# Optimization experiments

Hardware: AMD Instinct MI355X
Metric: run time of the kernel (lower is better)

The kernel has to match this reference:

```python
import jax, jax.numpy as jnp
import numpy as np

NHEADS = 16
RANK = 8


def _rope(t):
    # t: (B, H, S, hd); past_len = 0 (no kv cache)
    hd = t.shape[-1]
    S = t.shape[2]
    inv = 1.0 / (10000.0 ** (jnp.arange(0, hd, 2, dtype=jnp.float32) / hd))  # (hd/2,)
    ang = jnp.arange(S, dtype=jnp.float32)[:, None] * inv[None, :]           # (S, hd/2)
    cos = jnp.concatenate([jnp.cos(ang), jnp.cos(ang)], -1)[None, None]      # (1,1,S,hd)
    sin = jnp.concatenate([jnp.sin(ang), jnp.sin(ang)], -1)[None, None]
    t1, t2 = jnp.split(t, 2, axis=-1)
    rot = jnp.concatenate([-t2, t1], -1)
    return t * cos + rot * sin


def _hyper_linear(x, Ws, bs, w1, b1, w2, b2, gA_w, gA_b, gB_w, gB_b):
    # Static path + per-batch dynamic low-rank correction generated from pooled context.
    B, S, D = x.shape
    z = x.mean(axis=1)                              # (B, D) pooled context
    h = jax.nn.silu(z @ w1 + b1)                    # (B, D/ratio)
    c = h @ w2 + b2                                 # (B, dynamic_dim)
    A = (c @ gA_w + gA_b).reshape(B, RANK, D)       # (B, rank, D_in)
    Bm = (c @ gB_w + gB_b).reshape(B, D, RANK)      # (B, D_out, rank)
    xa = jnp.einsum('bsd,brd->bsr', x, A)           # (B, S, rank)
    dyn = jnp.einsum('bsr,bor->bso', xa, Bm) / RANK # (B, S, D_out)
    return x @ Ws + bs + dyn


def _forward(x, Wq, bq, Wo, bo,
             Wk, bk, k_w1, k_b1, k_w2, k_b2, k_gA_w, k_gA_b, k_gB_w, k_gB_b,
             Wv, bv, v_w1, v_b1, v_w2, v_b2, v_gA_w, v_gA_b, v_gB_w, v_gB_b):
    B, S, D = x.shape
    hd = D // NHEADS
    q = x @ Wq + bq
    k = _hyper_linear(x, Wk, bk, k_w1, k_b1, k_w2, k_b2, k_gA_w, k_gA_b, k_gB_w, k_gB_b)
    v = _hyper_linear(x, Wv, bv, v_w1, v_b1, v_w2, v_b2, v_gA_w, v_gA_b, v_gB_w, v_gB_b)
    # (B, S, D) -> (B, H, S, hd)
    q = q.reshape(B, S, NHEADS, hd).transpose(0, 2, 1, 3)
    k = k.reshape(B, S, NHEADS, hd).transpose(0, 2, 1, 3)
    v = v.reshape(B, S, NHEADS, hd).transpose(0, 2, 1, 3)
    q = _rope(q)
    k = _rope(k)
    # causal SDPA (kv_cache is None -> is_causal=True)
    scale = 1.0 / jnp.sqrt(jnp.asarray(hd, dtype=x.dtype))
    scores = jnp.einsum('bhqd,bhkd->bhqk', q, k) * scale
    mask = jnp.tril(jnp.ones((S, S), dtype=bool))
    scores = jnp.where(mask, scores, jnp.asarray(-1e30, dtype=scores.dtype))
    attn = jax.nn.softmax(scores, axis=-1)
    out = jnp.einsum('bhqk,bhkd->bhqd', attn, v)
    out = out.transpose(0, 2, 1, 3).reshape(B, S, D)
    return out @ Wo + bo


def setup_inputs() -> dict:
    key = jax.random.key(0)
    D, HID, DYN = 1024, 256, 64
    B, S = 2, 2048
    ks = jax.random.split(key, 32)
    w = lambda i, shp: jax.random.normal(ks[i], shp, dtype=jnp.float32) * 0.02
    inp = {
        'x': jax.random.normal(ks[0], (B, S, D), dtype=jnp.float32),
        'Wq': w(1, (D, D)), 'bq': jnp.zeros((D,), jnp.float32),
        'Wo': w(2, (D, D)), 'bo': jnp.zeros((D,), jnp.float32),
        'Wk': w(3, (D, D)), 'bk': jnp.zeros((D,), jnp.float32),
        'k_w1': w(4, (D, HID)), 'k_b1': jnp.zeros((HID,), jnp.float32),
        'k_w2': w(5, (HID, DYN)), 'k_b2': jnp.zeros((DYN,), jnp.float32),
        'k_gA_w': w(6, (DYN, RANK * D)), 'k_gA_b': jnp.zeros((RANK * D,), jnp.float32),
        'k_gB_w': w(7, (DYN, D * RANK)), 'k_gB_b': jnp.zeros((D * RANK,), jnp.float32),
        'Wv': w(8, (D, D)), 'bv': jnp.zeros((D,), jnp.float32),
        'v_w1': w(9, (D, HID)), 'v_b1': jnp.zeros((HID,), jnp.float32),
        'v_w2': w(10, (HID, DYN)), 'v_b2': jnp.zeros((DYN,), jnp.float32),
        'v_gA_w': w(11, (DYN, RANK * D)), 'v_gA_b': jnp.zeros((RANK * D,), jnp.float32),
        'v_gB_w': w(12, (DYN, D * RANK)), 'v_gB_b': jnp.zeros((D * RANK,), jnp.float32),
    }
    return inp


def reference(x, Wq, bq, Wo, bo,
              Wk, bk, k_w1, k_b1, k_w2, k_b2, k_gA_w, k_gA_b, k_gB_w, k_gB_b,
              Wv, bv, v_w1, v_b1, v_w2, v_b2, v_gA_w, v_gA_b, v_gB_w, v_gB_b):
    return _forward(x, Wq, bq, Wo, bo,
                    Wk, bk, k_w1, k_b1, k_w2, k_b2, k_gA_w, k_gA_b, k_gB_w, k_gB_b,
                    Wv, bv, v_w1, v_b1, v_w2, v_b2, v_gA_w, v_gA_b, v_gB_w, v_gB_b)
```

## Files before the change

kernel.cpp:

```cpp
#include <hip/hip_runtime.h>
#include <math.h>

#define BB 2
#define SS 2048
#define DD 1024
#define NH 16
#define HDM 64
#define RNK 8

typedef short short8 __attribute__((ext_vector_type(8)));
typedef float floatx4 __attribute__((ext_vector_type(4)));

static __device__ __forceinline__ ushort f2bf(float f) {
  union { float f; unsigned u; } v;
  v.f = f;
  unsigned r = (v.u + 0x7FFFu + ((v.u >> 16) & 1u)) >> 16;
  return (ushort)r;
}
static __device__ __forceinline__ float bf2f(ushort u) {
  union { unsigned u; float f; } v;
  v.u = ((unsigned)u) << 16;
  return v.f;
}

__global__ __launch_bounds__(256) void z_pool(const float* __restrict__ x,
                                              float* __restrict__ zsum) {
  int b = blockIdx.x;
  int s0 = blockIdx.y * 16;
  int tid = threadIdx.x;
  float p0 = 0.f, p1 = 0.f, p2 = 0.f, p3 = 0.f;
  const float* xp = x + ((size_t)b * SS + s0) * DD;
  for (int s = 0; s < 16; ++s) {
    const float* row = xp + (size_t)s * DD;
    p0 += row[tid];
    p1 += row[tid + 256];
    p2 += row[tid + 512];
    p3 += row[tid + 768];
  }
  atomicAdd(&zsum[b * DD + tid], p0);
  atomicAdd(&zsum[b * DD + tid + 256], p1);
  atomicAdd(&zsum[b * DD + tid + 512], p2);
  atomicAdd(&zsum[b * DD + tid + 768], p3);
}

__global__ __launch_bounds__(256) void gen_h(
    const float* __restrict__ zsum,
    const float* __restrict__ kw1, const float* __restrict__ vw1,
    float* __restrict__ h_pre) {
  int b = blockIdx.x & 1;
  int p = (blockIdx.x >> 1) & 1;
  int slice = blockIdx.y;
  const float* w1 = p ? vw1 : kw1;
  int tid = threadIdx.x;
  float acc = 0.f;
  int j0 = slice * 128;
  for (int j = j0; j < j0 + 128; ++j) {
    float z = zsum[b * DD + j] * (1.0f / (float)SS);
    acc += z * w1[j * 256 + tid];
  }
  atomicAdd(&h_pre[(p * 2 + b) * 256 + tid], acc);
}

__global__ __launch_bounds__(256) void hyper_c2(
    const float* __restrict__ h_pre,
    const float* __restrict__ kb1, const float* __restrict__ kw2,
    const float* __restrict__ kb2,
    const float* __restrict__ vb1, const float* __restrict__ vw2,
    const float* __restrict__ vb2, float* __restrict__ c_all) {
  int p = blockIdx.x >> 1;
  int b = blockIdx.x & 1;
  const float* b1 = p ? vb1 : kb1;
  const float* w2 = p ? vw2 : kw2;
  const float* b2 = p ? vb2 : kb2;
  __shared__ float hs[256];
  __shared__ float part[256];
  int tid = threadIdx.x;
  float hv = h_pre[(p * 2 + b) * 256 + tid] + b1[tid];
  hs[tid] = hv / (1.0f + expf(-hv));
  __syncthreads();
  int n = tid & 63, chunk = tid >> 6;
  float a = 0.f;
  for (int jj = 0; jj < 64; ++jj) {
    int j = chunk * 64 + jj;
    a += hs[j] * w2[j * 64 + n];
  }
  part[tid] = a;
  __syncthreads();
  if (tid < 64) {
    c_all[(p * 2 + b) * 64 + tid] =
        part[tid] + part[tid + 64] + part[tid + 128] + part[tid + 192] + b2[tid];
  }
}

__global__ __launch_bounds__(256) void gen_AB(
    const float* __restrict__ c_all,
    const float* __restrict__ kgAw, const float* __restrict__ kgAb,
    const float* __restrict__ kgBw, const float* __restrict__ kgBb,
    const float* __restrict__ vgAw, const float* __restrict__ vgAb,
    const float* __restrict__ vgBw, const float* __restrict__ vgBb,
    float* __restrict__ Ak, float* __restrict__ Bk,
    float* __restrict__ Av, float* __restrict__ Bv) {
  int y = blockIdx.y;
  int p = y >> 1, mat = y & 1;
  const float* gw = p ? (mat ? vgBw : vgAw) : (mat ? kgBw : kgAw);
  const float* gb = p ? (mat ? vgBb : vgAb) : (mat ? kgBb : kgAb);
  float* obase = p ? (mat ? Bv : Av) : (mat ? Bk : Ak);

  __shared__ float c0[64], c1[64];
  int tid = threadIdx.x;
  if (tid < 64) c0[tid] = c_all[p * 128 + tid];
  else if (tid < 128) c1[tid - 64] = c_all[p * 128 + tid];
  __syncthreads();

  int idx = blockIdx.x * 256 + tid;
  float a0 = gb[idx], a1 = a0;
#pragma unroll
  for (int j = 0; j < 64; ++j) {
    float w = gw[j * (RNK * DD) + idx];
    a0 += c0[j] * w;
    a1 += c1[j] * w;
  }
  obase[idx] = a0;
  obase[RNK * DD + idx] = a1;
}

__global__ __launch_bounds__(256) void cvt_bf16(const float* __restrict__ in,
                                                ushort* __restrict__ out) {
  int gid = blockIdx.x * 256 + threadIdx.x;
  float4 a = ((const float4*)in)[gid];
  ushort4 o;
  o.x = f2bf(a.x);
  o.y = f2bf(a.y);
  o.z = f2bf(a.z);
  o.w = f2bf(a.w);
  ((ushort4*)out)[gid] = o;
}

__global__ __launch_bounds__(256) void cvt_wt(const float* __restrict__ W,
                                              ushort* __restrict__ Wt) {
  __shared__ float tile[32][33];
  int bx = blockIdx.x, by = blockIdx.y;
  int tx = threadIdx.x & 31, ty = threadIdx.x >> 5;
#pragma unroll
  for (int i = 0; i < 4; ++i)
    tile[ty + 8 * i][tx] = W[(size_t)(by * 32 + ty + 8 * i) * DD + bx * 32 + tx];
  __syncthreads();
#pragma unroll
  for (int i = 0; i < 4; ++i)
    Wt[(size_t)(bx * 32 + ty + 8 * i) * DD + by * 32 + tx] =
        f2bf(tile[tx][ty + 8 * i]);
}

__global__ __launch_bounds__(256) void rope_tab(float2* __restrict__ tab) {
  int gid = blockIdx.x * 256 + threadIdx.x;
  int i = gid >> 11, s = gid & 2047;
  float freq = expf(-(float)i * (9.210340371976184f / 32.0f));
  float sn, cn;
  sincosf((float)s * freq, &sn, &cn);
  tab[gid] = make_float2(cn, sn);
}

__global__ __launch_bounds__(256) void weff(
    const float* __restrict__ Ak, const float* __restrict__ Bk,
    const float* __restrict__ Av, const float* __restrict__ Bv,
    const ushort* __restrict__ Wtk, const ushort* __restrict__ Wtv,
    ushort* __restrict__ Wcat) {
  int y = blockIdx.y;
  int p = y >> 1, b = y & 1;
  const float* A = (p ? Av : Ak) + b * (RNK * DD);
  const float* Bm = (p ? Bv : Bk) + b * (RNK * DD);
  const ushort* src = p ? Wtv : Wtk;
  ushort* dst = Wcat + ((size_t)(1 + 2 * p + b) << 20);

  int tid = threadIdx.x;
  int row = blockIdx.x * 16 + (tid >> 4);
  int cg = tid & 15;
  float bm[RNK];
#pragma unroll
  for (int r = 0; r < RNK; ++r) bm[r] = Bm[row * RNK + r];
  for (int kk = cg * 64; kk < cg * 64 + 64; kk += 4) {
    float4 acc = make_float4(0.f, 0.f, 0.f, 0.f);
#pragma unroll
    for (int r = 0; r < RNK; ++r) {
      float4 a4 = *(const float4*)&A[r * DD + kk];
      acc.x += bm[r] * a4.x;
      acc.y += bm[r] * a4.y;
      acc.z += bm[r] * a4.z;
      acc.w += bm[r] * a4.w;
    }
    ushort4 ws = *(const ushort4*)&src[(size_t)row * DD + kk];
    ushort4 o;
    o.x = f2bf(bf2f(ws.x) + acc.x * 0.125f);
    o.y = f2bf(bf2f(ws.y) + acc.y * 0.125f);
    o.z = f2bf(bf2f(ws.z) + acc.z * 0.125f);
    o.w = f2bf(bf2f(ws.w) + acc.w * 0.125f);
    *(ushort4*)&dst[(size_t)row * DD + kk] = o;
  }
}

__global__ __launch_bounds__(256) void gemm_qkv(
    const ushort* __restrict__ Axb, const ushort* __restrict__ Wcat,
    const float* __restrict__ bq, const float* __restrict__ bk,
    const float* __restrict__ bv, const float2* __restrict__ tab,
    ushort* __restrict__ qhb, ushort* __restrict__ khb,
    ushort* __restrict__ vhb) {
  __shared__ ushort As[128][40];
  __shared__ ushort Bs[128][40];
  int tid = threadIdx.x;
  int bm = blockIdx.x * 128;
  int ny = blockIdx.y;
  int path = ny >> 3;
  int nb = (ny & 7) * 128;
  int b_blk = bm >> 11;
  const ushort* Wbase =
      (path == 0) ? Wcat : Wcat + ((size_t)(1 + (path - 1) * 2 + b_blk) << 20);
  const float* bias = (path == 0) ? bq : (path == 1 ? bk : bv);
  ushort* outp = (path == 0) ? qhb : (path == 1 ? khb : vhb);

  int w = tid >> 6, lane = tid & 63, l16 = lane & 15, q4 = lane >> 4;
  int wm = (w >> 1) * 64, wn = (w & 1) * 64;
  floatx4 acc[4][4];
#pragma unroll
  for (int mi = 0; mi < 4; ++mi)
#pragma unroll
    for (int ni = 0; ni < 4; ++ni) acc[mi][ni] = 0;

  int sr = tid >> 2, sc = (tid & 3) * 8;
  const ushort* Ap0 = Axb + (size_t)(bm + sr) * DD + sc;
  const ushort* Ap1 = Axb + (size_t)(bm + sr + 64) * DD + sc;
  const ushort* Bp0 = Wbase + (size_t)(nb + sr) * DD + sc;
  const ushort* Bp1 = Wbase + (size_t)(nb + sr + 64) * DD + sc;

  for (int k0 = 0; k0 < DD; k0 += 32) {
    uint4 a0 = *(const uint4*)(Ap0 + k0);
    uint4 a1 = *(const uint4*)(Ap1 + k0);
    uint4 b0 = *(const uint4*)(Bp0 + k0);
    uint4 b1 = *(const uint4*)(Bp1 + k0);
    __syncthreads();
    *(uint4*)&As[sr][sc] = a0;
    *(uint4*)&As[sr + 64][sc] = a1;
    *(uint4*)&Bs[sr][sc] = b0;
    *(uint4*)&Bs[sr + 64][sc] = b1;
    __syncthreads();
    short8 af[4], bf[4];
#pragma unroll
    for (int mi = 0; mi < 4; ++mi)
      af[mi] = *(const short8*)&As[wm + mi * 16 + l16][q4 * 8];
#pragma unroll
    for (int ni = 0; ni < 4; ++ni)
      bf[ni] = *(const short8*)&Bs[wn + ni * 16 + l16][q4 * 8];
#pragma unroll
    for (int mi = 0; mi < 4; ++mi)
#pragma unroll
      for (int ni = 0; ni < 4; ++ni)
        acc[mi][ni] = __builtin_amdgcn_mfma_f32_16x16x32_bf16(
            af[mi], bf[ni], acc[mi][ni], 0, 0, 0);
  }

  int h = (nb + wn) >> 6;
  float biasv[4];
#pragma unroll
  for (int ni = 0; ni < 4; ++ni) biasv[ni] = bias[nb + wn + ni * 16 + l16];

#pragma unroll
  for (int mi = 0; mi < 4; ++mi) {
#pragma unroll
    for (int r = 0; r < 4; ++r) {
      int grow = bm + wm + mi * 16 + q4 * 4 + r;
      int bb = grow >> 11, s = grow & 2047;
      ushort* orow = outp + (((size_t)(bb * NH + h) * SS + s) << 6);
      float v[4];
#pragma unroll
      for (int ni = 0; ni < 4; ++ni) v[ni] = acc[mi][ni][r] + biasv[ni];
      if (path < 2) {
#pragma unroll
        for (int ni = 0; ni < 2; ++ni) {
          float2 cs = tab[((ni * 16 + l16) << 11) + s];
          float a = v[ni] * cs.x - v[ni + 2] * cs.y;
          float c = v[ni + 2] * cs.x + v[ni] * cs.y;
          v[ni] = a;
          v[ni + 2] = c;
        }
      }
#pragma unroll
      for (int ni = 0; ni < 4; ++ni) orow[ni * 16 + l16] = f2bf(v[ni]);
    }
  }
}

#define VT_IDX(d, c) ((unsigned)(72 * (d) + 16 * ((d) >> 3) + (c)))

__global__ __launch_bounds__(256) void attn_mfma2(
    const ushort* __restrict__ qh, const ushort* __restrict__ kh,
    const ushort* __restrict__ vh, ushort* __restrict__ ao) {
  __shared__ ushort Ks[64][72];
  __shared__ ushort Vt[4720];
  __shared__ ushort Ps[128][72];
  int bid = blockIdx.x;
  int bh = bid & 31;
  int q0 = (15 - (bid >> 5)) * 128;
  int b = bh >> 4, h = bh & 15;
  int tid = threadIdx.x;
  int w = tid >> 6, lane = tid & 63, l16 = lane & 15, q4 = lane >> 4;

  short8 qf[2][2];
#pragma unroll
  for (int mi = 0; mi < 2; ++mi) {
    const ushort* qrow =
        qh + ((size_t)bh * SS + q0 + 32 * w + mi * 16 + l16) * HDM;
    qf[mi][0] = *(const short8*)(qrow + q4 * 8);
    qf[mi][1] = *(const short8*)(qrow + 32 + q4 * 8);
  }

  floatx4 o[2][4];
#pragma unroll
  for (int mi = 0; mi < 2; ++mi)
#pragma unroll
    for (int ni = 0; ni < 4; ++ni) o[mi][ni] = 0;
  float l_part[2][4] = {};

  int nkt = (q0 >> 6) + 2;
  int skr = tid >> 2, skc = (tid & 3) * 8;
  int so8 = tid & 7, sp = tid >> 3;
  const ushort* kbase = kh + (size_t)bh * SS * HDM;
  const ushort* vbase = vh + (size_t)bh * SS * HDM;

  for (int kt = 0; kt < nkt; ++kt) {
    int k0 = kt * 64;
    __syncthreads();
    *(uint4*)&Ks[skr][skc] =
        *(const uint4*)(kbase + (size_t)(k0 + skr) * HDM + skc);
    *(uint4*)&Ks[skr][skc + 32] =
        *(const uint4*)(kbase + (size_t)(k0 + skr) * HDM + skc + 32);
    const ushort* v0 = vbase + (size_t)(k0 + 2 * sp) * HDM + so8 * 8;
    uint4 va = *(const uint4*)v0;
    uint4 vb = *(const uint4*)(v0 + HDM);
    const ushort* pa = (const ushort*)&va;
    const ushort* pb = (const ushort*)&vb;
#pragma unroll
    for (int j = 0; j < 8; ++j) {
      int d = so8 * 8 + j;
      *(unsigned*)&Vt[VT_IDX(d, 2 * sp)] =
          (unsigned)pa[j] | ((unsigned)pb[j] << 16);
    }
    __syncthreads();

    floatx4 s4[2][4];
#pragma unroll
    for (int ni = 0; ni < 4; ++ni) {
      short8 kf0 = *(const short8*)&Ks[ni * 16 + l16][q4 * 8];
      short8 kf1 = *(const short8*)&Ks[ni * 16 + l16][32 + q4 * 8];
#pragma unroll
      for (int mi = 0; mi < 2; ++mi) {
        floatx4 c;
        c = 0;
        c = __builtin_amdgcn_mfma_f32_16x16x32_bf16(qf[mi][0], kf0, c, 0, 0, 0);
        c = __builtin_amdgcn_mfma_f32_16x16x32_bf16(qf[mi][1], kf1, c, 0, 0, 0);
        s4[mi][ni] = c;
      }
    }

    bool diag = (kt >= nkt - 2);
#pragma unroll
    for (int mi = 0; mi < 2; ++mi) {
#pragma unroll
      for (int r = 0; r < 4; ++r) {
        int qg = q0 + 32 * w + mi * 16 + q4 * 4 + r;
        int prow = 32 * w + mi * 16 + q4 * 4 + r;
        float lp = 0.f;
#pragma unroll
        for (int ni = 0; ni < 4; ++ni) {
          float t = s4[mi][ni][r] * 0.18033688f;
          if (diag && (k0 + ni * 16 + l16) > qg) t = -1e38f;
          float p = exp2f(t);
          lp += p;
          Ps[prow][ni * 16 + l16] = f2bf(p);
        }
        l_part[mi][r] += lp;
      }
    }

    short8 pf[2][2];
#pragma unroll
    for (int mi = 0; mi < 2; ++mi) {
      pf[mi][0] = *(const short8*)&Ps[32 * w + mi * 16 + l16][q4 * 8];
      pf[mi][1] = *(const short8*)&Ps[32 * w + mi * 16 + l16][32 + q4 * 8];
    }
#pragma unroll
    for (int ni = 0; ni < 4; ++ni) {
      short8 vf0 = *(const short8*)&Vt[VT_IDX(ni * 16 + l16, q4 * 8)];
      short8 vf1 = *(const short8*)&Vt[VT_IDX(ni * 16 + l16, 32 + q4 * 8)];
#pragma unroll
      for (int mi = 0; mi < 2; ++mi) {
        o[mi][ni] =
            __builtin_amdgcn_mfma_f32_16x16x32_bf16(pf[mi][0], vf0, o[mi][ni], 0, 0, 0);
        o[mi][ni] =
            __builtin_amdgcn_mfma_f32_16x16x32_bf16(pf[mi][1], vf1, o[mi][ni], 0, 0, 0);
      }
    }
  }

#pragma unroll
  for (int mi = 0; mi < 2; ++mi) {
#pragma unroll
    for (int r = 0; r < 4; ++r) {
      float l = l_part[mi][r];
      l += __shfl_xor(l, 1);
      l += __shfl_xor(l, 2);
      l += __shfl_xor(l, 4);
      l += __shfl_xor(l, 8);
      float inv = 1.0f / l;
      int token = q0 + 32 * w + mi * 16 + q4 * 4 + r;
      ushort* orow = ao + ((size_t)(b * SS + token)) * DD + h * HDM;
#pragma unroll
      for (int ni = 0; ni < 4; ++ni)
        orow[ni * 16 + l16] = f2bf(o[mi][ni][r] * inv);
    }
  }
}

__global__ __launch_bounds__(256) void gemm_out(
    const ushort* __restrict__ A, const ushort* __restrict__ Bt,
    const float* __restrict__ bias, float* __restrict__ C) {
  __shared__ ushort As[64][40];
  __shared__ ushort Bs[128][40];
  int tid = threadIdx.x;
  int bm = blockIdx.x * 64, bn = blockIdx.y * 128;
  int w = tid >> 6, lane = tid & 63, l16 = lane & 15, q4 = lane >> 4;
  int wm = (w >> 1) * 32, wn = (w & 1) * 64;
  floatx4 acc[2][4];
#pragma unroll
  for (int mi = 0; mi < 2; ++mi)
#pragma unroll
    for (int ni = 0; ni < 4; ++ni) acc[mi][ni] = 0;

  int sr = tid >> 2, sc = (tid & 3) * 8;
  const ushort* Ap0 = A + (size_t)(bm + sr) * DD + sc;
  const ushort* Bp0 = Bt + (size_t)(bn + sr) * DD + sc;
  const ushort* Bp1 = Bt + (size_t)(bn + sr + 64) * DD + sc;

  for (int k0 = 0; k0 < DD; k0 += 32) {
    uint4 a0 = *(const uint4*)(Ap0 + k0);
    uint4 b0 = *(const uint4*)(Bp0 + k0);
    uint4 b1 = *(const uint4*)(Bp1 + k0);
    __syncthreads();
    *(uint4*)&As[sr & 63][sc] = a0;
    *(uint4*)&Bs[sr][sc] = b0;
    *(uint4*)&Bs[sr + 64][sc] = b1;
    __syncthreads();
    short8 af[2], bf[4];
#pragma unroll
    for (int mi = 0; mi < 2; ++mi)
      af[mi] = *(const short8*)&As[wm + mi * 16 + l16][q4 * 8];
#pragma unroll
    for (int ni = 0; ni < 4; ++ni)
      bf[ni] = *(const short8*)&Bs[wn + ni * 16 + l16][q4 * 8];
#pragma unroll
    for (int mi = 0; mi < 2; ++mi)
#pragma unroll
      for (int ni = 0; ni < 4; ++ni)
        acc[mi][ni] = __builtin_amdgcn_mfma_f32_16x16x32_bf16(
            af[mi], bf[ni], acc[mi][ni], 0, 0, 0);
  }
#pragma unroll
  for (int mi = 0; mi < 2; ++mi) {
#pragma unroll
    for (int r = 0; r < 4; ++r) {
      int row = bm + wm + mi * 16 + q4 * 4 + r;
      float* Cr = C + (size_t)row * DD;
#pragma unroll
      for (int ni = 0; ni < 4; ++ni) {
        int col = bn + wn + ni * 16 + l16;
        Cr[col] = acc[mi][ni][r] + bias[col];
      }
    }
  }
}

extern "C" void kernel_launch(void* const* d_in, const int* in_sizes, int n_in,
                              void* d_out, int out_size, void* d_ws,
                              size_t ws_size, hipStream_t stream) {
  const float* x    = (const float*)d_in[0];
  const float* Wq   = (const float*)d_in[1];
  const float* bq   = (const float*)d_in[2];
  const float* Wo   = (const float*)d_in[3];
  const float* bo   = (const float*)d_in[4];
  const float* Wk   = (const float*)d_in[5];
  const float* bk   = (const float*)d_in[6];
  const float* kw1  = (const float*)d_in[7];
  const float* kb1  = (const float*)d_in[8];
  const float* kw2  = (const float*)d_in[9];
  const float* kb2  = (const float*)d_in[10];
  const float* kgAw = (const float*)d_in[11];
  const float* kgAb = (const float*)d_in[12];
  const float* kgBw = (const float*)d_in[13];
  const float* kgBb = (const float*)d_in[14];
  const float* Wv   = (const float*)d_in[15];
  const float* bv   = (const float*)d_in[16];
  const float* vw1  = (const float*)d_in[17];
  const float* vb1  = (const float*)d_in[18];
  const float* vw2  = (const float*)d_in[19];
  const float* vb2  = (const float*)d_in[20];
  const float* vgAw = (const float*)d_in[21];
  const float* vgAb = (const float*)d_in[22];
  const float* vgBw = (const float*)d_in[23];
  const float* vgBb = (const float*)d_in[24];
  float* out = (float*)d_out;

  char* ws = (char*)d_ws;
  const size_t MB = 1024 * 1024;
  ushort* qhb  = (ushort*)(ws);
  ushort* khb  = (ushort*)(ws + 8 * MB);
  ushort* vhb  = (ushort*)(ws + 16 * MB);
  ushort* xb   = (ushort*)(ws + 24 * MB);
  ushort* aob  = (ushort*)(ws + 32 * MB);
  ushort* Wcat = (ushort*)(ws + 40 * MB);
  ushort* Wto  = (ushort*)(ws + 50 * MB);
  ushort* Wtk  = (ushort*)(ws + 52 * MB);
  ushort* Wtv  = (ushort*)(ws + 54 * MB);
  float*  Ak   = (float*)(ws + 56 * MB);
  float*  Bk   = Ak + BB * RNK * DD;
  float*  Av   = Bk + BB * RNK * DD;
  float*  Bv   = Av + BB * RNK * DD;
  float*  zsum = Bv + BB * RNK * DD;
  float*  h_pre = zsum + BB * DD;
  float*  c_all = h_pre + 4 * 256;
  float2* tab  = (float2*)(ws + 56 * MB + 512 * 1024);

  hipMemsetAsync(zsum, 0, (BB * DD + 4 * 256) * sizeof(float), stream);
  z_pool<<<dim3(BB, SS / 16), 256, 0, stream>>>(x, zsum);
  gen_h<<<dim3(4, 8), 256, 0, stream>>>(zsum, kw1, vw1, h_pre);
  hyper_c2<<<4, 256, 0, stream>>>(h_pre, kb1, kw2, kb2, vb1, vw2, vb2, c_all);
  gen_AB<<<dim3(RNK * DD / 256, 4), 256, 0, stream>>>(
      c_all, kgAw, kgAb, kgBw, kgBb, vgAw, vgAb, vgBw, vgBb, Ak, Bk, Av, Bv);

  cvt_bf16<<<(BB * SS * DD / 4) / 256, 256, 0, stream>>>(x, xb);
  cvt_wt<<<dim3(32, 32), 256, 0, stream>>>(Wq, Wcat);
  cvt_wt<<<dim3(32, 32), 256, 0, stream>>>(Wk, Wtk);
  cvt_wt<<<dim3(32, 32), 256, 0, stream>>>(Wv, Wtv);
  cvt_wt<<<dim3(32, 32), 256, 0, stream>>>(Wo, Wto);
  rope_tab<<<(32 * 2048) / 256, 256, 0, stream>>>(tab);
  weff<<<dim3(64, 4), 256, 0, stream>>>(Ak, Bk, Av, Bv, Wtk, Wtv, Wcat);

  gemm_qkv<<<dim3(32, 24), 256, 0, stream>>>(xb, Wcat, bq, bk, bv, tab, qhb,
                                             khb, vhb);
  attn_mfma2<<<512, 256, 0, stream>>>(qhb, khb, vhb, aob);
  gemm_out<<<dim3(64, 8), 256, 0, stream>>>(aob, Wto, bo, out);
}
```

Before: 335.4 us.

## Rewrite attention kernel with 64-row tiles, register K, and double-buffered V

Replaces the attention kernel with a 128-thread version over 64-query tiles, launching twice as many blocks. K fragments now load straight into registers and V goes into a double-buffered transposed LDS tile, with the next tile prefetched during compute so there is one barrier per iteration instead of two. The MFMA operands are swapped (K·Q, V·P) so results land in a layout that allows packed P and output stores. P is rounded to bf16 by truncation rather than round-to-nearest, which adds a small precision risk.

```diff
diff --git a/kernel.cpp b/kernel.cpp
--- a/kernel.cpp
+++ b/kernel.cpp
@@ -21,6 +21,20 @@
   union { unsigned u; float f; } v;
   v.u = ((unsigned)u) << 16;
   return v.f;
+}
+static __device__ __forceinline__ unsigned pack_bf_trunc(float a, float b) {
+  union { float f; unsigned u; } x, y;
+  x.f = a;
+  y.f = b;
+  return __builtin_amdgcn_perm(y.u, x.u, 0x07060302u);
+}
+static __device__ __forceinline__ unsigned pack_bf_rne(float a, float b) {
+  union { float f; unsigned u; } x, y;
+  x.f = a;
+  y.f = b;
+  unsigned xu = x.u + 0x7FFFu + ((x.u >> 16) & 1u);
+  unsigned yu = y.u + 0x7FFFu + ((y.u >> 16) & 1u);
+  return __builtin_amdgcn_perm(yu, xu, 0x07060302u);
 }
 
 __global__ __launch_bounds__(256) void z_pool(const float* __restrict__ x,
@@ -290,131 +304,170 @@
 
 #define VT_IDX(d, c) ((unsigned)(72 * (d) + 16 * ((d) >> 3) + (c)))
 
-__global__ __launch_bounds__(256) void attn_mfma2(
+__global__ __launch_bounds__(128) void attn_mfma3(
     const ushort* __restrict__ qh, const ushort* __restrict__ kh,
     const ushort* __restrict__ vh, ushort* __restrict__ ao) {
-  __shared__ ushort Ks[64][72];
-  __shared__ ushort Vt[4720];
-  __shared__ ushort Ps[128][72];
+  __shared__ ushort Ps[64][72];
+  __shared__ ushort Vt[2][4720];
   int bid = blockIdx.x;
   int bh = bid & 31;
-  int q0 = (15 - (bid >> 5)) * 128;
+  int q0 = (31 - (bid >> 5)) * 64;
   int b = bh >> 4, h = bh & 15;
   int tid = threadIdx.x;
   int w = tid >> 6, lane = tid & 63, l16 = lane & 15, q4 = lane >> 4;
-
-  short8 qf[2][2];
-#pragma unroll
-  for (int mi = 0; mi < 2; ++mi) {
-    const ushort* qrow =
-        qh + ((size_t)bh * SS + q0 + 32 * w + mi * 16 + l16) * HDM;
-    qf[mi][0] = *(const short8*)(qrow + q4 * 8);
-    qf[mi][1] = *(const short8*)(qrow + 32 + q4 * 8);
-  }
-
-  floatx4 o[2][4];
-#pragma unroll
-  for (int mi = 0; mi < 2; ++mi)
-#pragma unroll
-    for (int ni = 0; ni < 4; ++ni) o[mi][ni] = 0;
-  float l_part[2][4] = {};
-
-  int nkt = (q0 >> 6) + 2;
-  int skr = tid >> 2, skc = (tid & 3) * 8;
-  int so8 = tid & 7, sp = tid >> 3;
+  int nkt = (q0 >> 6) + 1;
+
   const ushort* kbase = kh + (size_t)bh * SS * HDM;
   const ushort* vbase = vh + (size_t)bh * SS * HDM;
 
+  short8 qf[2][2];
+#pragma unroll
+  for (int qi = 0; qi < 2; ++qi) {
+    const ushort* qrow = qh + ((size_t)bh * SS + q0 + 32 * w + 16 * qi + l16) * HDM;
+    qf[qi][0] = *(const short8*)(qrow + 8 * q4);
+    qf[qi][1] = *(const short8*)(qrow + 32 + 8 * q4);
+  }
+
+  int so8 = tid & 7, sp = (tid >> 3) & 15;
+
+  short8 kf[4][2];
+#pragma unroll
+  for (int ki = 0; ki < 4; ++ki) {
+    const ushort* kr = kbase + (size_t)(16 * ki + l16) * HDM + 8 * q4;
+    kf[ki][0] = *(const short8*)(kr);
+    kf[ki][1] = *(const short8*)(kr + 32);
+  }
+  uint4 vr[4];
+#pragma unroll
+  for (int j = 0; j < 4; ++j)
+    vr[j] = *(const uint4*)(vbase + (size_t)(4 * sp + j) * HDM + 8 * so8);
+#pragma unroll
+  for (int j = 0; j < 4; j += 2) {
+    const ushort* pa = (const ushort*)&vr[j];
+    const ushort* pb = (const ushort*)&vr[j + 1];
+#pragma unroll
+    for (int dd = 0; dd < 8; ++dd) {
+      int d = so8 * 8 + dd;
+      *(unsigned*)&Vt[0][VT_IDX(d, 4 * sp + j)] =
+          (unsigned)pa[dd] | ((unsigned)pb[dd] << 16);
+    }
+  }
+  __syncthreads();
+
+  floatx4 o[4][2];
+#pragma unroll
+  for (int di = 0; di < 4; ++di)
+#pragma unroll
+    for (int qi = 0; qi < 2; ++qi) o[di][qi] = 0;
+  float l_part[2] = {0.f, 0.f};
+
   for (int kt = 0; kt < nkt; ++kt) {
-    int k0 = kt * 64;
-    __syncthreads();
-    *(uint4*)&Ks[skr][skc] =
-        *(const uint4*)(kbase + (size_t)(k0 + skr) * HDM + skc);
-    *(uint4*)&Ks[skr][skc + 32] =
-        *(const uint4*)(kbase + (size_t)(k0 + skr) * HDM + skc + 32);
-    const ushort* v0 = vbase + (size_t)(k0 + 2 * sp) * HDM + so8 * 8;
-    uint4 va = *(const uint4*)v0;
-    uint4 vb = *(const uint4*)(v0 + HDM);
-    const ushort* pa = (const ushort*)&va;
-    const ushort* pb = (const ushort*)&vb;
-#pragma unroll
-    for (int j = 0; j < 8; ++j) {
-      int d = so8 * 8 + j;
-      *(unsigned*)&Vt[VT_IDX(d, 2 * sp)] =
-          (unsigned)pa[j] | ((unsigned)pb[j] << 16);
-    }
-    __syncthreads();
+    int buf = kt & 1;
+    bool has_next = (kt + 1) < nkt;
+    short8 kn[4][2];
+    if (has_next) {
+      int k0n = (kt + 1) * 64;
+#pragma unroll
+      for (int ki = 0; ki < 4; ++ki) {
+        const ushort* kr = kbase + (size_t)(k0n + 16 * ki + l16) * HDM + 8 * q4;
+        kn[ki][0] = *(const short8*)(kr);
+        kn[ki][1] = *(const short8*)(kr + 32);
+      }
+#pragma unroll
+      for (int j = 0; j < 4; ++j)
+        vr[j] = *(const uint4*)(vbase + (size_t)(k0n + 4 * sp + j) * HDM + 8 * so8);
+    }
 
     floatx4 s4[2][4];
 #pragma unroll
-    for (int ni = 0; ni < 4; ++ni) {
-      short8 kf0 = *(const short8*)&Ks[ni * 16 + l16][q4 * 8];
-      short8 kf1 = *(const short8*)&Ks[ni * 16 + l16][32 + q4 * 8];
-#pragma unroll
-      for (int mi = 0; mi < 2; ++mi) {
+    for (int ki = 0; ki < 4; ++ki)
+#pragma unroll
+      for (int qi = 0; qi < 2; ++qi) {
         floatx4 c;
         c = 0;
-        c = __builtin_amdgcn_mfma_f32_16x16x32_bf16(qf[mi][0], kf0, c, 0, 0, 0);
-        c = __builtin_amdgcn_mfma_f32_16x16x32_bf16(qf[mi][1], kf1, c, 0, 0, 0);
-        s4[mi][ni] = c;
-      }
-    }
-
-    bool diag = (kt >= nkt - 2);
-#pragma unroll
-    for (int mi = 0; mi < 2; ++mi) {
-#pragma unroll
-      for (int r = 0; r < 4; ++r) {
-        int qg = q0 + 32 * w + mi * 16 + q4 * 4 + r;
-        int prow = 32 * w + mi * 16 + q4 * 4 + r;
-        float lp = 0.f;
-#pragma unroll
-        for (int ni = 0; ni < 4; ++ni) {
-          float t = s4[mi][ni][r] * 0.18033688f;
-          if (diag && (k0 + ni * 16 + l16) > qg) t = -1e38f;
-          float p = exp2f(t);
-          lp += p;
-          Ps[prow][ni * 16 + l16] = f2bf(p);
+        c = __builtin_amdgcn_mfma_f32_16x16x32_bf16(kf[ki][0], qf[qi][0], c, 0, 0, 0);
+        c = __builtin_amdgcn_mfma_f32_16x16x32_bf16(kf[ki][1], qf[qi][1], c, 0, 0, 0);
+        s4[qi][ki] = c;
+      }
+
+    bool diag = (kt == nkt - 1);
+#pragma unroll
+    for (int qi = 0; qi < 2; ++qi) {
+      int qloc = 32 * w + 16 * qi + l16;
+      float lp = 0.f;
+#pragma unroll
+      for (int ki = 0; ki < 4; ++ki) {
+        float p[4];
+#pragma unroll
+        for (int r = 0; r < 4; ++r) {
+          float t = s4[qi][ki][r] * 0.18033688f;
+          float pv = exp2f(t);
+          if (diag && (16 * ki + 4 * q4 + r) > qloc) pv = 0.f;
+          p[r] = pv;
+          lp += pv;
         }
-        l_part[mi][r] += lp;
-      }
-    }
-
-    short8 pf[2][2];
-#pragma unroll
-    for (int mi = 0; mi < 2; ++mi) {
-      pf[mi][0] = *(const short8*)&Ps[32 * w + mi * 16 + l16][q4 * 8];
-      pf[mi][1] = *(const short8*)&Ps[32 * w + mi * 16 + l16][32 + q4 * 8];
-    }
-#pragma unroll
-    for (int ni = 0; ni < 4; ++ni) {
-      short8 vf0 = *(const short8*)&Vt[VT_IDX(ni * 16 + l16, q4 * 8)];
-      short8 vf1 = *(const short8*)&Vt[VT_IDX(ni * 16 + l16, 32 + q4 * 8)];
-#pragma unroll
-      for (int mi = 0; mi < 2; ++mi) {
-        o[mi][ni] =
-            __builtin_amdgcn_mfma_f32_16x16x32_bf16(pf[mi][0], vf0, o[mi][ni], 0, 0, 0);
-        o[mi][ni] =
-            __builtin_amdgcn_mfma_f32_16x16x32_bf16(pf[mi][1], vf1, o[mi][ni], 0, 0, 0);
-      }
-    }
-  }
-
-#pragma unroll
-  for (int mi = 0; mi < 2; ++mi) {
-#pragma unroll
-    for (int r = 0; r < 4; ++r) {
-      float l = l_part[mi][r];
-      l += __shfl_xor(l, 1);
-      l += __shfl_xor(l, 2);
-      l += __shfl_xor(l, 4);
-      l += __shfl_xor(l, 8);
-      float inv = 1.0f / l;
-      int token = q0 + 32 * w + mi * 16 + q4 * 4 + r;
-      ushort* orow = ao + ((size_t)(b * SS + token)) * DD + h * HDM;
-#pragma unroll
-      for (int ni = 0; ni < 4; ++ni)
-        orow[ni * 16 + l16] = f2bf(o[mi][ni][r] * inv);
+        unsigned u0 = pack_bf_trunc(p[0], p[1]);
+        unsigned u1 = pack_bf_trunc(p[2], p[3]);
+        uint2 u2;
+        u2.x = u0;
+        u2.y = u1;
+        *(uint2*)&Ps[qloc][16 * ki + 4 * q4] = u2;
+      }
+      l_part[qi] += lp;
+    }
+
+#pragma unroll
+    for (int qi = 0; qi < 2; ++qi) {
+      short8 pf0 = *(const short8*)&Ps[32 * w + 16 * qi + l16][8 * q4];
+      short8 pf1 = *(const short8*)&Ps[32 * w + 16 * qi + l16][32 + 8 * q4];
+#pragma unroll
+      for (int di = 0; di < 4; ++di) {
+        short8 vf0 = *(const short8*)&Vt[buf][VT_IDX(16 * di + l16, 8 * q4)];
+        short8 vf1 = *(const short8*)&Vt[buf][VT_IDX(16 * di + l16, 32 + 8 * q4)];
+        o[di][qi] =
+            __builtin_amdgcn_mfma_f32_16x16x32_bf16(vf0, pf0, o[di][qi], 0, 0, 0);
+        o[di][qi] =
+            __builtin_amdgcn_mfma_f32_16x16x32_bf16(vf1, pf1, o[di][qi], 0, 0, 0);
+      }
+    }
+
+    if (has_next) {
+      int nb = (kt + 1) & 1;
+#pragma unroll
+      for (int j = 0; j < 4; j += 2) {
+        const ushort* pa = (const ushort*)&vr[j];
+        const ushort* pb = (const ushort*)&vr[j + 1];
+#pragma unroll
+        for (int dd = 0; dd < 8; ++dd) {
+          int d = so8 * 8 + dd;
+          *(unsigned*)&Vt[nb][VT_IDX(d, 4 * sp + j)] =
+              (unsigned)pa[dd] | ((unsigned)pb[dd] << 16);
+        }
+      }
+#pragma unroll
+      for (int ki = 0; ki < 4; ++ki) {
+        kf[ki][0] = kn[ki][0];
+        kf[ki][1] = kn[ki][1];
+      }
+    }
+    __syncthreads();
+  }
+
+#pragma unroll
+  for (int qi = 0; qi < 2; ++qi) {
+    float l = l_part[qi];
+    l += __shfl_xor(l, 16);
+    l += __shfl_xor(l, 32);
+    float inv = 1.0f / l;
+    int token = q0 + 32 * w + 16 * qi + l16;
+    ushort* orow = ao + ((size_t)(b * SS + token)) * DD + h * HDM;
+#pragma unroll
+    for (int di = 0; di < 4; ++di) {
+      floatx4 ov = o[di][qi];
+      uint2 u2;
+      u2.x = pack_bf_rne(ov[0] * inv, ov[1] * inv);
+      u2.y = pack_bf_rne(ov[2] * inv, ov[3] * inv);
+      *(uint2*)&orow[16 * di + 4 * q4] = u2;
     }
   }
 }
@@ -544,6 +597,6 @@
 
   gemm_qkv<<<dim3(32, 24), 256, 0, stream>>>(xb, Wcat, bq, bk, bv, tab, qhb,
                                              khb, vhb);
-  attn_mfma2<<<512, 256, 0, stream>>>(qhb, khb, vhb, aob);
+  attn_mfma3<<<1024, 128, 0, stream>>>(qhb, khb, vhb, aob);
   gemm_out<<<dim3(64, 8), 256, 0, stream>>>(aob, Wto, bo, out);
 }
```

Result: faster. 325.0 us (-3.1%).
